# Optimization experiments

Hardware: AMD Instinct MI355X
Metric: run time of the kernel (lower is better)

The kernel has to match this reference:

```python
import jax, jax.numpy as jnp
import numpy as np

EMBED = 512
H = 8
HD = EMBED // H           # 64
NUM_CLS = 4
WIN = 32                  # one-sided window radius
DIL = 1
WLEN = 2 * WIN + 1        # 65
CTX = NUM_CLS + WLEN      # 69
PATCH_LEN = 8192
B = 1
S = NUM_CLS + PATCH_LEN
THETA = 10000.0
COORD_HIGH = 100000.0
NEG = -1e30


def _rotate_half(x):
    # [..., x1, x2, ...] -> [..., -x2, x1, ...]
    x1 = x[..., 0::2]
    x2 = x[..., 1::2]
    return jnp.stack([-x2, x1], axis=-1).reshape(x.shape)


def _rope2d(x, coords):
    # x: (B,H,L,HD), coords: (B,L,2)
    half = HD // 2
    inv_freq = 1.0 / (THETA ** (jnp.arange(0, half, 2, dtype=jnp.float32) / half))  # (half//2,)
    xy = coords / COORD_HIGH
    fx = xy[..., 0][..., None] * inv_freq   # (B,L,half//2)
    fy = xy[..., 1][..., None] * inv_freq
    fx = jnp.repeat(fx, 2, axis=-1)         # (B,L,half)
    fy = jnp.repeat(fy, 2, axis=-1)
    freqs = jnp.concatenate([fx, fy], axis=-1)[:, None]  # (B,1,L,HD)
    return x * jnp.cos(freqs) + _rotate_half(x) * jnp.sin(freqs)


def setup_inputs() -> dict:
    key = jax.random.key(0)
    k1, k2, k3, k4, k5, k6 = jax.random.split(key, 6)
    x = jax.random.normal(k1, (B, S, EMBED), dtype=jnp.float32)
    coords = jax.random.uniform(k2, (B, PATCH_LEN, 2), dtype=jnp.float32) * COORD_HIGH
    sc = 1.0 / np.sqrt(EMBED)
    w_qkv = jax.random.normal(k3, (3 * EMBED, EMBED), dtype=jnp.float32) * sc
    b_qkv = jax.random.normal(k4, (3 * EMBED,), dtype=jnp.float32) * 0.02
    w_out = jax.random.normal(k5, (EMBED, EMBED), dtype=jnp.float32) * sc
    b_out = jax.random.normal(k6, (EMBED,), dtype=jnp.float32) * 0.02
    return {"x": x, "coords": coords, "w_qkv": w_qkv, "b_qkv": b_qkv,
            "w_out": w_out, "b_out": b_out}


def _forward(x, coords, w_qkv, b_qkv, w_out, b_out):
    Bb, seq_len, _ = x.shape
    qkv = x @ w_qkv.T + b_qkv                       # (B,S,3E)
    qkv = qkv.reshape(Bb, seq_len, 3, H, HD)
    qkv = jnp.transpose(qkv, (2, 0, 3, 1, 4))       # (3,B,H,S,HD)
    q, k, v = qkv[0], qkv[1], qkv[2]
    q_cls, k_cls, v_cls = q[:, :, :NUM_CLS], k[:, :, :NUM_CLS], v[:, :, :NUM_CLS]
    q_p, k_p, v_p = q[:, :, NUM_CLS:], k[:, :, NUM_CLS:], v[:, :, NUM_CLS:]

    q_p = _rope2d(q_p, coords)
    k_p = _rope2d(k_p, coords)
    k_all = jnp.concatenate([k_cls, k_p], axis=2)
    v_all = v

    scale = 1.0 / np.sqrt(HD)

    # --- global CLS attention: CLS queries attend to everything ---
    cls_scores = jnp.einsum('bhqd,bhkd->bhqk', q_cls, k_all) * scale
    cls_probs = jax.nn.softmax(cls_scores, axis=-1)
    cls_out = jnp.einsum('bhqk,bhkd->bhqd', cls_probs, v_all)

    # --- windowed patch attention: patch i -> [CLS | patches i-W..i+W (dilated)] ---
    L = PATCH_LEN
    pad = WIN * DIL
    k_pad = jnp.pad(k_p, ((0, 0), (0, 0), (pad, pad), (0, 0)))
    v_pad = jnp.pad(v_p, ((0, 0), (0, 0), (pad, pad), (0, 0)))
    gather_idx = jnp.arange(L)[:, None] + jnp.arange(WLEN)[None, :] * DIL  # (L,WLEN)
    k_win = k_pad[:, :, gather_idx]   # (B,H,L,WLEN,HD)
    v_win = v_pad[:, :, gather_idx]

    s_cls = jnp.einsum('bhld,bhcd->bhlc', q_p, k_cls) * scale     # (B,H,L,NUM_CLS)
    s_win = jnp.einsum('bhld,bhlwd->bhlw', q_p, k_win) * scale    # (B,H,L,WLEN)

    pos = jnp.arange(L)[:, None] + (jnp.arange(WLEN)[None, :] - WIN) * DIL
    in_bounds = (pos >= 0) & (pos < L)                            # (L,WLEN)
    s_win = jnp.where(in_bounds[None, None], s_win, NEG)

    scores = jnp.concatenate([s_cls, s_win], axis=-1)             # (B,H,L,CTX)
    probs = jax.nn.softmax(scores, axis=-1)
    p_cls, p_win = probs[..., :NUM_CLS], probs[..., NUM_CLS:]
    patch_out = (jnp.einsum('bhlc,bhcd->bhld', p_cls, v_cls)
                 + jnp.einsum('bhlw,bhlwd->bhld', p_win, v_win))

    out = jnp.concatenate([cls_out, patch_out], axis=2)           # (B,H,S,HD)
    out = jnp.transpose(out, (0, 2, 1, 3)).reshape(Bb, seq_len, EMBED)
    return out @ w_out.T + b_out


def reference(x, coords, w_qkv, b_qkv, w_out, b_out):
    return _forward(x, coords, w_qkv, b_qkv, w_out, b_out)
```

## Files before the change

### kernel.cpp

```cpp
#include <hip/hip_runtime.h>
#include <math.h>

#define EMBED 512
#define NHEAD 8
#define HD 64
#define NUM_CLS 4
#define WIN 32
#define WLEN 65
#define PATCH_LEN 8192
#define S_TOT 8196
#define QKV_LD 1536
#define VT_LD 8200

typedef short bf16x8 __attribute__((ext_vector_type(8)));
typedef float f32x4 __attribute__((ext_vector_type(4)));

__device__ __forceinline__ unsigned short f2bf(float f) {
    unsigned u = __float_as_uint(f);
    return (unsigned short)((u + 0x7fffu + ((u >> 16) & 1u)) >> 16);
}
__device__ __forceinline__ float bf2f(unsigned short v) {
    return __uint_as_float((unsigned)v << 16);
}
__device__ __forceinline__ void gll16(const unsigned short* g, unsigned short* l) {
    __builtin_amdgcn_global_load_lds((const __attribute__((address_space(1))) void*)g,
                                     (__attribute__((address_space(3))) void*)l, 16, 0, 0);
}

__global__ __launch_bounds__(256) void cast_all(const float* __restrict__ x,
                                                const float* __restrict__ wq,
                                                const float* __restrict__ wo,
                                                unsigned short* __restrict__ xb,
                                                unsigned short* __restrict__ wqb,
                                                unsigned short* __restrict__ wob)
{
    const int n1 = S_TOT * EMBED;
    const int n2 = 3 * EMBED * EMBED;
    const int n3 = EMBED * EMBED;
    const int i = (blockIdx.x * 256 + threadIdx.x) * 4;
    const float* src;
    unsigned short* dst;
    int j;
    if (i < n1)           { src = x;  dst = xb;  j = i; }
    else if (i < n1 + n2) { src = wq; dst = wqb; j = i - n1; }
    else if (i < n1 + n2 + n3) { src = wo; dst = wob; j = i - n1 - n2; }
    else return;
    const float4 v = *(const float4*)(src + j);
    ushort4 o;
    o.x = f2bf(v.x); o.y = f2bf(v.y); o.z = f2bf(v.z); o.w = f2bf(v.w);
    *(ushort4*)(dst + j) = o;
}

#define EXW 136
__global__ __launch_bounds__(256) void gemm_qkv(const unsigned short* __restrict__ A,
                                                const unsigned short* __restrict__ B,
                                                const float* __restrict__ bias,
                                                unsigned short* __restrict__ C,
                                                const float* __restrict__ coords,
                                                unsigned short* __restrict__ vT)
{
    const int M = S_TOT, N = 3 * EMBED, K = EMBED;
    __shared__ __align__(16) unsigned short SMEM[16384];
    unsigned short* EX = SMEM;

    const int tid = threadIdx.x;
    const int lane = tid & 63, w = tid >> 6;
    const int xcd = blockIdx.x & 7;
    const int s = blockIdx.x >> 3;
    const int bm = xcd + 8 * (s / 12);
    const int bn = s % 12;
    if (bm >= 65) return;

    const int ar0 = tid >> 2;
    const int col8 = (tid & 3) * 8;
    int gm0 = bm * 128 + ar0;       if (gm0 >= M) gm0 = M - 1;
    int gm1 = bm * 128 + ar0 + 64;  if (gm1 >= M) gm1 = M - 1;
    const unsigned short* pa0 = A + (size_t)gm0 * K + col8;
    const unsigned short* pa1 = A + (size_t)gm1 * K + col8;
    const unsigned short* pb0 = B + (size_t)(bn * 128 + ar0) * K + col8;
    const unsigned short* pb1 = B + (size_t)(bn * 128 + ar0 + 64) * K + col8;

    const int wr = (w & 1) * 64;
    const int wc = (w >> 1) * 64;
    const int fr = lane & 15;
    const int fk = (lane >> 4) * 8;

    f32x4 acc[4][4];
#pragma unroll
    for (int mi = 0; mi < 4; ++mi)
#pragma unroll
        for (int ni = 0; ni < 4; ++ni) acc[mi][ni] = (f32x4)0.f;

    gll16(pa0, SMEM + tid * 8);
    gll16(pa1, SMEM + (tid + 256) * 8);
    gll16(pb0, SMEM + 8192 + tid * 8);
    gll16(pb1, SMEM + 8192 + (tid + 256) * 8);

    for (int it = 0; it < 16; ++it) {
        __syncthreads();
        if (it + 1 < 16) {
            const int k0 = (it + 1) * 32;
            const int off = ((it + 1) & 1) * 4096;
            gll16(pa0 + k0, SMEM + off + tid * 8);
            gll16(pa1 + k0, SMEM + off + (tid + 256) * 8);
            gll16(pb0 + k0, SMEM + 8192 + off + tid * 8);
            gll16(pb1 + k0, SMEM + 8192 + off + (tid + 256) * 8);
        }
        const unsigned short* Asb = SMEM + (it & 1) * 4096;
        const unsigned short* Bsb = SMEM + 8192 + (it & 1) * 4096;
        bf16x8 af[4], bf[4];
#pragma unroll
        for (int mi = 0; mi < 4; ++mi)
            af[mi] = *(const bf16x8*)(Asb + (wr + mi * 16 + fr) * 32 + fk);
#pragma unroll
        for (int ni = 0; ni < 4; ++ni)
            bf[ni] = *(const bf16x8*)(Bsb + (wc + ni * 16 + fr) * 32 + fk);
#pragma unroll
        for (int mi = 0; mi < 4; ++mi)
#pragma unroll
            for (int ni = 0; ni < 4; ++ni)
                acc[mi][ni] = __builtin_amdgcn_mfma_f32_16x16x32_bf16(af[mi], bf[ni], acc[mi][ni], 0, 0, 0);
    }
    __syncthreads();

    const int ccol = bn * 128 + wc + fr;

    if (bn < 8) {
        ushort2* rt = (ushort2*)EX;
        for (int idx = tid; idx < 4096; idx += 256) {
            const int rr = idx >> 5, pr = idx & 31;
            int l = bm * 128 + rr - NUM_CLS;
            l = l < 0 ? 0 : (l > PATCH_LEN - 1 ? PATCH_LEN - 1 : l);
            const float cxy = coords[l * 2 + (pr >> 4)] * 1e-5f;
            const float f = cxy * __expf(-(float)(pr & 15) * 0.5756462732485114f);
            float sn, cs;
            __sincosf(f, &sn, &cs);
            ushort2 e; e.x = f2bf(cs); e.y = f2bf(sn);
            rt[idx] = e;
        }
        __syncthreads();

        unsigned pv[4][4][2];
#pragma unroll
        for (int mi = 0; mi < 4; ++mi) {
#pragma unroll
            for (int r = 0; r < 4; ++r) {
                const int rloc = wr + mi * 16 + (lane >> 4) * 4 + r;
                const int row = bm * 128 + rloc;
                const bool patch = (row >= NUM_CLS) && (row < M);
#pragma unroll
                for (int ni = 0; ni < 4; ++ni) {
                    const int col = ccol + ni * 16;
                    const float biased = acc[mi][ni][r] + bias[col];
                    const float prt = __shfl_xor(biased, 1);
                    float outv = biased;
                    if (patch) {
                        const ushort2 e = rt[rloc * 32 + ((col & 63) >> 1)];
                        const float cs = bf2f(e.x), sn = bf2f(e.y);
                        outv = (col & 1) ? (biased * cs + prt * sn)
                                         : (biased * cs - prt * sn);
                    }
                    const unsigned us = f2bf(outv);
                    if (r & 1) pv[mi][ni][r >> 1] |= us << 16;
                    else       pv[mi][ni][r >> 1] = us;
                }
            }
        }
        for (int p = 0; p < 2; ++p) {
            __syncthreads();
            if ((w & 1) == p) {
#pragma unroll
                for (int mi = 0; mi < 4; ++mi) {
#pragma unroll
                    for (int r = 0; r < 4; ++r) {
                        const int rl = mi * 16 + (lane >> 4) * 4 + r;
#pragma unroll
                        for (int ni = 0; ni < 4; ++ni) {
                            const unsigned pw = pv[mi][ni][r >> 1];
                            EX[rl * EXW + wc + fr + ni * 16] =
                                (unsigned short)((r & 1) ? (pw >> 16) : (pw & 0xffff));
                        }
                    }
                }
            }
            __syncthreads();
#pragma unroll
            for (int i = 0; i < 4; ++i) {
                const int idx = tid + 256 * i;
                const int rowl = idx >> 4, ch = idx & 15;
                const int grow = bm * 128 + p * 64 + rowl;
                if (grow < M)
                    *(bf16x8*)(C + (size_t)grow * N + bn * 128 + ch * 8) =
                        *(const bf16x8*)(EX + rowl * EXW + ch * 8);
            }
        }
    } else {
        const int dbase = (bn - 8) * 128;
#pragma unroll
        for (int mi = 0; mi < 4; ++mi) {
            const int rbase = bm * 128 + wr + mi * 16 + (lane >> 4) * 4;
#pragma unroll
            for (int ni = 0; ni < 4; ++ni) {
                const int col = ccol + ni * 16;
#pragma unroll
                for (int r = 0; r < 4; ++r) {
                    const int row = rbase + r;
                    if (row < M)
                        C[(size_t)row * N + col] = f2bf(acc[mi][ni][r] + bias[col]);
                }
            }
        }
        for (int p = 0; p < 2; ++p) {
            __syncthreads();
            if ((w >> 1) == p) {
#pragma unroll
                for (int mi = 0; mi < 4; ++mi) {
                    const int tok0 = wr + mi * 16 + (lane >> 4) * 4;
                    const int rw = bm * 128 + tok0;
#pragma unroll
                    for (int ni = 0; ni < 4; ++ni) {
                        const int col = ccol + ni * 16;
                        const int dloc = fr + 16 * ni;
                        ushort4 o;
                        o.x = (rw + 0 < M) ? f2bf(acc[mi][ni][0] + bias[col]) : (unsigned short)0;
                        o.y = (rw + 1 < M) ? f2bf(acc[mi][ni][1] + bias[col]) : (unsigned short)0;
                        o.z = (rw + 2 < M) ? f2bf(acc[mi][ni][2] + bias[col]) : (unsigned short)0;
                        o.w = (rw + 3 < M) ? f2bf(acc[mi][ni][3] + bias[col]) : (unsigned short)0;
                        *(ushort4*)(EX + dloc * EXW + tok0) = o;
                    }
                }
            }
            __syncthreads();
            const int d = tid >> 2;
            const int tch = (tid & 3) * 32;
            const int gtok = bm * 128 + tch;
            unsigned short* dst = vT + (size_t)(dbase + p * 64 + d) * VT_LD + gtok;
            const unsigned short* srcl = EX + d * EXW + tch;
            if (gtok + 32 <= VT_LD) {
#pragma unroll
                for (int c2 = 0; c2 < 32; c2 += 8)
                    *(bf16x8*)(dst + c2) = *(const bf16x8*)(srcl + c2);
            } else {
                for (int c2 = 0; c2 < 32; ++c2)
                    if (gtok + c2 < VT_LD) dst[c2] = srcl[c2];
            }
        }
    }
}

__global__ __launch_bounds__(256) void gemm_out(const unsigned short* __restrict__ A,
                                                const unsigned short* __restrict__ B,
                                                const float* __restrict__ bias,
                                                float* __restrict__ C)
{
    const int M = S_TOT, N = EMBED, K = EMBED;
    __shared__ __align__(16) unsigned short As[2][64 * 32];
    __shared__ __align__(16) unsigned short Bs[2][128 * 32];
    const int tid = threadIdx.x;
    const int lane = tid & 63, w = tid >> 6;
    const int bn = blockIdx.x, bm = blockIdx.y;

    const int ar0 = tid >> 2;
    const int col8 = (tid & 3) * 8;
    int gm0 = bm * 64 + ar0;  if (gm0 >= M) gm0 = M - 1;
    const unsigned short* pa0 = A + (size_t)gm0 * K + col8;
    const unsigned short* pb0 = B + (size_t)(bn * 128 + ar0) * K + col8;
    const unsigned short* pb1 = B + (size_t)(bn * 128 + ar0 + 64) * K + col8;

    const int wr = (w & 1) * 32;
    const int wc = (w >> 1) * 64;
    const int fr = lane & 15;
    const int fk = (lane >> 4) * 8;

    f32x4 acc[2][4];
#pragma unroll
    for (int mi = 0; mi < 2; ++mi)
#pragma unroll
        for (int ni = 0; ni < 4; ++ni) acc[mi][ni] = (f32x4)0.f;

    gll16(pa0, As[0] + tid * 8);
    gll16(pb0, Bs[0] + tid * 8);
    gll16(pb1, Bs[0] + (tid + 256) * 8);

    for (int it = 0; it < 16; ++it) {
        __syncthreads();
        if (it + 1 < 16) {
            const int k0 = (it + 1) * 32;
            const int nb = (it + 1) & 1;
            gll16(pa0 + k0, As[nb] + tid * 8);
            gll16(pb0 + k0, Bs[nb] + tid * 8);
            gll16(pb1 + k0, Bs[nb] + (tid + 256) * 8);
        }
        const int cb = it & 1;
        bf16x8 af[2], bf[4];
#pragma unroll
        for (int mi = 0; mi < 2; ++mi)
            af[mi] = *(const bf16x8*)(As[cb] + (wr + mi * 16 + fr) * 32 + fk);
#pragma unroll
        for (int ni = 0; ni < 4; ++ni)
            bf[ni] = *(const bf16x8*)(Bs[cb] + (wc + ni * 16 + fr) * 32 + fk);
#pragma unroll
        for (int mi = 0; mi < 2; ++mi)
#pragma unroll
            for (int ni = 0; ni < 4; ++ni)
                acc[mi][ni] = __builtin_amdgcn_mfma_f32_16x16x32_bf16(af[mi], bf[ni], acc[mi][ni], 0, 0, 0);
    }

    const int ccol = bn * 128 + wc + fr;
#pragma unroll
    for (int mi = 0; mi < 2; ++mi) {
        const int rbase = bm * 64 + wr + mi * 16 + (lane >> 4) * 4;
#pragma unroll
        for (int r = 0; r < 4; ++r) {
            const int row = rbase + r;
            if (row < M) {
#pragma unroll
                for (int ni = 0; ni < 4; ++ni)
                    C[(size_t)row * N + ccol + ni * 16] = acc[mi][ni][r] + bias[ccol + ni * 16];
            }
        }
    }
}

#define CCH 128
#define NCHUNK ((S_TOT + CCH - 1) / CCH)
#define PSTRIDE 68

__global__ __launch_bounds__(256) void cls_attn_partial(const unsigned short* __restrict__ qkv,
                                                        float* __restrict__ part)
{
    const int h = blockIdx.x;
    const int c = blockIdx.y;
    const int tid = threadIdx.x;
    const int base = c * CCH;

    __shared__ float qs[4][64];
    __shared__ __align__(16) unsigned short Kl[128 * 64];
    __shared__ float sc[4][CCH];
    __shared__ float ored[4][4][64];
    __shared__ float ml[4][2];

    {
        const int qi = tid >> 6, d = tid & 63;
        qs[qi][d] = bf2f(qkv[(size_t)qi * QKV_LD + h * HD + d]);
    }
    for (int i = tid; i < 1024; i += 256) {
        const int kr = i >> 3;
        const int dc = (i & 7) ^ (kr & 7);
        int j = base + kr; if (j > S_TOT - 1) j = S_TOT - 1;
        gll16(qkv + (size_t)j * QKV_LD + EMBED + h * HD + dc * 8, Kl + i * 8);
    }
    __syncthreads();

    {
        const int jj = tid & 127;
        const int qp = (tid >> 7) * 2;
        const int j = base + jj;
        float s0 = -INFINITY, s1 = -INFINITY;
        if (j < S_TOT) {
            float a0 = 0.f, a1 = 0.f;
#pragma unroll
            for (int cch = 0; cch < 8; ++cch) {
                const int slot = cch ^ (jj & 7);
                const bf16x8 kv8 = *(const bf16x8*)(Kl + jj * 64 + slot * 8);
#pragma unroll
                for (int u = 0; u < 8; ++u) {
                    const float kf = bf2f((unsigned short)kv8[u]);
                    a0 += qs[qp + 0][cch * 8 + u] * kf;
                    a1 += qs[qp + 1][cch * 8 + u] * kf;
                }
            }
            s0 = a0 * 0.125f; s1 = a1 * 0.125f;
        }
        sc[qp + 0][jj] = s0;
        sc[qp + 1][jj] = s1;
    }
    __syncthreads();

    const int w = tid >> 6, lane = tid & 63;
    {
        float m = fmaxf(sc[w][lane], sc[w][lane + 64]);
#pragma unroll
        for (int off = 32; off > 0; off >>= 1) m = fmaxf(m, __shfl_xor(m, off, 64));
        const float e0 = expf(sc[w][lane] - m);
        const float e1 = expf(sc[w][lane + 64] - m);
        sc[w][lane] = e0; sc[w][lane + 64] = e1;
        float lsum = e0 + e1;
#pragma unroll
        for (int off = 32; off > 0; off >>= 1) lsum += __shfl_xor(lsum, off, 64);
        if (lane == 0) { ml[w][0] = m; ml[w][1] = lsum; }
    }
    __syncthreads();

    {
        const int g = w, d = lane;
        float a0 = 0.f, a1 = 0.f, a2 = 0.f, a3 = 0.f;
        for (int jj = g; jj < CCH; jj += 4) {
            const int j = base + jj;
            if (j >= S_TOT) break;
            const float vv = bf2f(qkv[(size_t)j * QKV_LD + 2 * EMBED + h * HD + d]);
            a0 += sc[0][jj] * vv; a1 += sc[1][jj] * vv;
            a2 += sc[2][jj] * vv; a3 += sc[3][jj] * vv;
        }
        ored[g][0][d] = a0; ored[g][1][d] = a1; ored[g][2][d] = a2; ored[g][3][d] = a3;
    }
    __syncthreads();

    {
        const int qi = tid >> 6, d = tid & 63;
        const float o = ored[0][qi][d] + ored[1][qi][d] + ored[2][qi][d] + ored[3][qi][d];
        float* pb = part + ((size_t)(h * NCHUNK + c) * 4 + qi) * PSTRIDE;
        pb[d] = o;
        if (d == 0) { pb[64] = ml[qi][0]; pb[65] = ml[qi][1]; }
    }
}

__global__ __launch_bounds__(256) void cls_attn_combine(const float* __restrict__ part,
                                                        unsigned short* __restrict__ attn)
{
    const int h = blockIdx.x;
    const int qi = threadIdx.x >> 6, d = threadIdx.x & 63;
    float M = -INFINITY;
    for (int c = 0; c < NCHUNK; ++c)
        M = fmaxf(M, part[((size_t)(h * NCHUNK + c) * 4 + qi) * PSTRIDE + 64]);
    float acc = 0.f, L = 0.f;
    for (int c = 0; c < NCHUNK; ++c) {
        const float* pb = part + ((size_t)(h * NCHUNK + c) * 4 + qi) * PSTRIDE;
        const float s = expf(pb[64] - M);
        acc += s * pb[d];
        L   += s * pb[65];
    }
    attn[(size_t)qi * EMBED + h * HD + d] = f2bf(acc / L);
}

#define SW 116
#define PW 136

__global__ __launch_bounds__(256) void patch_attn_mfma(
    const unsigned short* __restrict__ qkv,
    const unsigned short* __restrict__ vT,
    unsigned short* __restrict__ attnb)
{
    const int l0 = blockIdx.x * 32;
    const int h = blockIdx.y;
    const int tid = threadIdx.x;
    const int lane = tid & 63, w = tid >> 6;

    __shared__ __align__(16) unsigned short Qs[32 * 64];
    __shared__ __align__(16) unsigned short Ks[112 * 64];
    __shared__ __align__(16) unsigned short Vt[64 * 128];
    __shared__ __align__(16) float Sm[32 * SW];

    {
        const int i = tid;
        const int t = i >> 3;
        const int dcl = (i & 7) ^ (t & 7);
        gll16(qkv + (size_t)(NUM_CLS + l0 + t) * QKV_LD + h * HD + dcl * 8, Qs + i * 8);
    }
    for (int i = tid; i < 896; i += 256) {
        const int c = i >> 3;
        const int dcl = (i & 7) ^ (c & 7);
        int tok = (c >= 104 && c < 108) ? (c - 104) : (l0 - 32 + c);
        tok = tok < 0 ? 0 : (tok > S_TOT - 1 ? S_TOT - 1 : tok);
        gll16(qkv + (size_t)tok * QKV_LD + EMBED + h * HD + dcl * 8, Ks + i * 8);
    }
    for (int i = tid; i < 1024; i += 256) {
        const int d = i >> 4;
        const int kcl = (i & 15) ^ (d & 15);
        const int c0 = kcl * 8;
        int tokb = (c0 == 104) ? 0 : (l0 - 32 + c0);
        tokb = tokb < 0 ? 0 : (tokb > 8192 ? 8192 : tokb);
        gll16(vT + (size_t)(h * HD + d) * VT_LD + tokb, Vt + i * 8);
    }
    __syncthreads();

    bf16x8 qf[2][2];
#pragma unroll
    for (int mt = 0; mt < 2; ++mt)
#pragma unroll
        for (int ks = 0; ks < 2; ++ks) {
            const int row = mt * 16 + (lane & 15);
            const int dc = (ks * 4 + (lane >> 4)) ^ (row & 7);
            qf[mt][ks] = *(const bf16x8*)(Qs + row * 64 + dc * 8);
        }
    for (int idx = w; idx < 14; idx += 4) {
        const int mt = idx & 1, nt = idx >> 1;
        f32x4 acc = (f32x4)0.f;
#pragma unroll
        for (int ks = 0; ks < 2; ++ks) {
            const int kr = nt * 16 + (lane & 15);
            const int dc = (ks * 4 + (lane >> 4)) ^ (kr & 7);
            const bf16x8 kf = *(const bf16x8*)(Ks + kr * 64 + dc * 8);
            acc = __builtin_amdgcn_mfma_f32_16x16x32_bf16(qf[mt][ks], kf, acc, 0, 0, 0);
        }
        const int col = nt * 16 + (lane & 15);
        const int r0 = mt * 16 + (lane >> 4) * 4;
#pragma unroll
        for (int r = 0; r < 4; ++r) Sm[(r0 + r) * SW + col] = acc[r];
    }
    __syncthreads();

    {
        const int t = tid >> 3, lq = tid & 7;
        float e[14];
        float m = -INFINITY;
#pragma unroll
        for (int j = 0; j < 14; ++j) {
            const int c = lq + 8 * j;
            bool valid;
            if (c >= 104) valid = (c < 108);
            else {
                const int r = c - 4;
                const int pos = l0 - 32 + r;
                valid = (c >= 4) && (c < 100) && (r >= t) && (r <= t + 64) &&
                        (pos >= 0) && (pos < PATCH_LEN);
            }
            e[j] = valid ? Sm[t * SW + c] * 0.125f : -INFINITY;
            m = fmaxf(m, e[j]);
        }
#pragma unroll
        for (int off = 1; off < 8; off <<= 1) m = fmaxf(m, __shfl_xor(m, off, 64));
        float sum = 0.f;
#pragma unroll
        for (int j = 0; j < 14; ++j) { e[j] = expf(e[j] - m); sum += e[j]; }
#pragma unroll
        for (int off = 1; off < 8; off <<= 1) sum += __shfl_xor(sum, off, 64);
        const float inv = 1.f / sum;
        __syncthreads();
        unsigned short* P = (unsigned short*)Sm;
#pragma unroll
        for (int j = 0; j < 14; ++j) P[t * PW + lq + 8 * j] = f2bf(e[j] * inv);
        ushort2 z; z.x = 0; z.y = 0;
        *(ushort2*)(P + (tid >> 3) * PW + 112 + (tid & 7) * 2) = z;
    }
    __syncthreads();

    {
        const unsigned short* P = (const unsigned short*)Sm;
        const int mt = w & 1;
        bf16x8 pf[4];
#pragma unroll
        for (int ks = 0; ks < 4; ++ks) {
            const int row = mt * 16 + (lane & 15);
            pf[ks] = *(const bf16x8*)(P + row * PW + ks * 32 + (lane >> 4) * 8);
        }
#pragma unroll
        for (int nn = 0; nn < 2; ++nn) {
            const int nt = (w >> 1) + nn * 2;
            f32x4 acc = (f32x4)0.f;
#pragma unroll
            for (int ks = 0; ks < 4; ++ks) {
                const int d = nt * 16 + (lane & 15);
                const int kc = (ks * 4 + (lane >> 4)) ^ (d & 15);
                const bf16x8 vf = *(const bf16x8*)(Vt + d * 128 + kc * 8);
                acc = __builtin_amdgcn_mfma_f32_16x16x32_bf16(pf[ks], vf, acc, 0, 0, 0);
            }
            const int dcol = nt * 16 + (lane & 15);
            const int r0 = mt * 16 + (lane >> 4) * 4;
#pragma unroll
            for (int r = 0; r < 4; ++r)
                attnb[(size_t)(NUM_CLS + l0 + r0 + r) * EMBED + h * HD + dcol] = f2bf(acc[r]);
        }
    }
}

extern "C" void kernel_launch(void* const* d_in, const int* in_sizes, int n_in,
                              void* d_out, int out_size, void* d_ws, size_t ws_size,
                              hipStream_t stream)
{
    const float* x      = (const float*)d_in[0];
    const float* coords = (const float*)d_in[1];
    const float* w_qkv  = (const float*)d_in[2];
    const float* b_qkv  = (const float*)d_in[3];
    const float* w_out  = (const float*)d_in[4];
    const float* b_out  = (const float*)d_in[5];
    float* out = (float*)d_out;

    char* p = (char*)d_ws;
    unsigned short* qkv   = (unsigned short*)p;  p += (size_t)S_TOT * QKV_LD * 2;
    unsigned short* vT    = (unsigned short*)p;  p += (size_t)EMBED * VT_LD * 2;
    unsigned short* attnb = (unsigned short*)p;  p += (size_t)S_TOT * EMBED * 2;
    float*          part  = (float*)p;           p += (size_t)NHEAD * NCHUNK * 4 * PSTRIDE * 4;
    unsigned short* wob   = (unsigned short*)p;  p += (size_t)EMBED * EMBED * 2;
    unsigned short* xb    = (unsigned short*)p;  p += (size_t)S_TOT * EMBED * 2;
    unsigned short* wqb   = (unsigned short*)p;


    {
        const int total = S_TOT * EMBED + 3 * EMBED * EMBED + EMBED * EMBED;
        cast_all<<<(total / 4 + 255) / 256, 256, 0, stream>>>(x, w_qkv, w_out, xb, wqb, wob);
    }

    gemm_qkv<<<864, 256, 0, stream>>>(xb, wqb, b_qkv, qkv, coords, vT);

    cls_attn_partial<<<dim3(NHEAD, NCHUNK), 256, 0, stream>>>(qkv, part);
    cls_attn_combine<<<NHEAD, 256, 0, stream>>>(part, attnb);

    patch_attn_mfma<<<dim3(PATCH_LEN / 32, NHEAD), 256, 0, stream>>>(qkv, vT, attnb);

    gemm_out<<<dim3(4, 129), 256, 0, stream>>>(attnb, wob, b_out, out);
}
```

Baseline: 185.0 us.

## Fuse x bf16 cast into QKV GEMM and merge cls/patch attention launches

The QKV GEMM now reads fp32 x directly, converts it to bf16 in registers and stores it to LDS after the MFMAs. This removes the separate cast pass over x and its bf16 workspace copy, but the A loads become register-staged instead of async LDS loads. The patch-attention and cls-partial kernels are merged into one launch with a block-index split, cutting one launch and letting both run concurrently. Weights are still cast in a smaller kernel.

```diff
diff --git a/kernel.cpp b/kernel.cpp
--- a/kernel.cpp
+++ b/kernel.cpp
@@ -26,24 +26,28 @@
     __builtin_amdgcn_global_load_lds((const __attribute__((address_space(1))) void*)g,
                                      (__attribute__((address_space(3))) void*)l, 16, 0, 0);
 }
-
-__global__ __launch_bounds__(256) void cast_all(const float* __restrict__ x,
-                                                const float* __restrict__ wq,
-                                                const float* __restrict__ wo,
-                                                unsigned short* __restrict__ xb,
-                                                unsigned short* __restrict__ wqb,
-                                                unsigned short* __restrict__ wob)
+__device__ __forceinline__ bf16x8 pack8(float4 lo, float4 hi) {
+    bf16x8 r;
+    r[0] = (short)f2bf(lo.x); r[1] = (short)f2bf(lo.y);
+    r[2] = (short)f2bf(lo.z); r[3] = (short)f2bf(lo.w);
+    r[4] = (short)f2bf(hi.x); r[5] = (short)f2bf(hi.y);
+    r[6] = (short)f2bf(hi.z); r[7] = (short)f2bf(hi.w);
+    return r;
+}
+
+__global__ __launch_bounds__(256) void cast_w(const float* __restrict__ wq,
+                                              const float* __restrict__ wo,
+                                              unsigned short* __restrict__ wqb,
+                                              unsigned short* __restrict__ wob)
 {
-    const int n1 = S_TOT * EMBED;
     const int n2 = 3 * EMBED * EMBED;
     const int n3 = EMBED * EMBED;
     const int i = (blockIdx.x * 256 + threadIdx.x) * 4;
     const float* src;
     unsigned short* dst;
     int j;
-    if (i < n1)           { src = x;  dst = xb;  j = i; }
-    else if (i < n1 + n2) { src = wq; dst = wqb; j = i - n1; }
-    else if (i < n1 + n2 + n3) { src = wo; dst = wob; j = i - n1 - n2; }
+    if (i < n2)           { src = wq; dst = wqb; j = i; }
+    else if (i < n2 + n3) { src = wo; dst = wob; j = i - n2; }
     else return;
     const float4 v = *(const float4*)(src + j);
     ushort4 o;
@@ -52,7 +56,7 @@
 }
 
 #define EXW 136
-__global__ __launch_bounds__(256) void gemm_qkv(const unsigned short* __restrict__ A,
+__global__ __launch_bounds__(256) void gemm_qkv(const float* __restrict__ X,
                                                 const unsigned short* __restrict__ B,
                                                 const float* __restrict__ bias,
                                                 unsigned short* __restrict__ C,
@@ -75,8 +79,8 @@
     const int col8 = (tid & 3) * 8;
     int gm0 = bm * 128 + ar0;       if (gm0 >= M) gm0 = M - 1;
     int gm1 = bm * 128 + ar0 + 64;  if (gm1 >= M) gm1 = M - 1;
-    const unsigned short* pa0 = A + (size_t)gm0 * K + col8;
-    const unsigned short* pa1 = A + (size_t)gm1 * K + col8;
+    const float* Xp0 = X + (size_t)gm0 * K + col8;
+    const float* Xp1 = X + (size_t)gm1 * K + col8;
     const unsigned short* pb0 = B + (size_t)(bn * 128 + ar0) * K + col8;
     const unsigned short* pb1 = B + (size_t)(bn * 128 + ar0 + 64) * K + col8;
 
@@ -91,20 +95,30 @@
 #pragma unroll
         for (int ni = 0; ni < 4; ++ni) acc[mi][ni] = (f32x4)0.f;
 
-    gll16(pa0, SMEM + tid * 8);
-    gll16(pa1, SMEM + (tid + 256) * 8);
-    gll16(pb0, SMEM + 8192 + tid * 8);
-    gll16(pb1, SMEM + 8192 + (tid + 256) * 8);
+    {
+        const float4 a00 = *(const float4*)(Xp0);
+        const float4 a01 = *(const float4*)(Xp0 + 4);
+        const float4 a10 = *(const float4*)(Xp1);
+        const float4 a11 = *(const float4*)(Xp1 + 4);
+        gll16(pb0, SMEM + 8192 + tid * 8);
+        gll16(pb1, SMEM + 8192 + (tid + 256) * 8);
+        *(bf16x8*)(SMEM + tid * 8) = pack8(a00, a01);
+        *(bf16x8*)(SMEM + (tid + 256) * 8) = pack8(a10, a11);
+    }
 
     for (int it = 0; it < 16; ++it) {
         __syncthreads();
-        if (it + 1 < 16) {
-            const int k0 = (it + 1) * 32;
+        float4 n00, n01, n10, n11;
+        const bool more = (it + 1 < 16);
+        if (more) {
+            const int kf = (it + 1) * 32;
+            n00 = *(const float4*)(Xp0 + kf);
+            n01 = *(const float4*)(Xp0 + kf + 4);
+            n10 = *(const float4*)(Xp1 + kf);
+            n11 = *(const float4*)(Xp1 + kf + 4);
             const int off = ((it + 1) & 1) * 4096;
-            gll16(pa0 + k0, SMEM + off + tid * 8);
-            gll16(pa1 + k0, SMEM + off + (tid + 256) * 8);
-            gll16(pb0 + k0, SMEM + 8192 + off + tid * 8);
-            gll16(pb1 + k0, SMEM + 8192 + off + (tid + 256) * 8);
+            gll16(pb0 + kf, SMEM + 8192 + off + tid * 8);
+            gll16(pb1 + kf, SMEM + 8192 + off + (tid + 256) * 8);
         }
         const unsigned short* Asb = SMEM + (it & 1) * 4096;
         const unsigned short* Bsb = SMEM + 8192 + (it & 1) * 4096;
@@ -120,6 +134,11 @@
 #pragma unroll
             for (int ni = 0; ni < 4; ++ni)
                 acc[mi][ni] = __builtin_amdgcn_mfma_f32_16x16x32_bf16(af[mi], bf[ni], acc[mi][ni], 0, 0, 0);
+        if (more) {
+            const int off = ((it + 1) & 1) * 4096;
+            *(bf16x8*)(SMEM + off + tid * 8) = pack8(n00, n01);
+            *(bf16x8*)(SMEM + off + (tid + 256) * 8) = pack8(n10, n11);
+        }
     }
     __syncthreads();
 
@@ -325,93 +344,223 @@
 #define CCH 128
 #define NCHUNK ((S_TOT + CCH - 1) / CCH)
 #define PSTRIDE 68
-
-__global__ __launch_bounds__(256) void cls_attn_partial(const unsigned short* __restrict__ qkv,
-                                                        float* __restrict__ part)
+#define SW 116
+#define PW 136
+
+__global__ __launch_bounds__(256) void attn_fused(
+    const unsigned short* __restrict__ qkv,
+    const unsigned short* __restrict__ vT,
+    float* __restrict__ part,
+    unsigned short* __restrict__ attnb)
 {
-    const int h = blockIdx.x;
-    const int c = blockIdx.y;
+    __shared__ __align__(16) char SM[49664];
     const int tid = threadIdx.x;
-    const int base = c * CCH;
-
-    __shared__ float qs[4][64];
-    __shared__ __align__(16) unsigned short Kl[128 * 64];
-    __shared__ float sc[4][CCH];
-    __shared__ float ored[4][4][64];
-    __shared__ float ml[4][2];
-
-    {
-        const int qi = tid >> 6, d = tid & 63;
-        qs[qi][d] = bf2f(qkv[(size_t)qi * QKV_LD + h * HD + d]);
-    }
-    for (int i = tid; i < 1024; i += 256) {
-        const int kr = i >> 3;
-        const int dc = (i & 7) ^ (kr & 7);
-        int j = base + kr; if (j > S_TOT - 1) j = S_TOT - 1;
-        gll16(qkv + (size_t)j * QKV_LD + EMBED + h * HD + dc * 8, Kl + i * 8);
-    }
-    __syncthreads();
-
-    {
-        const int jj = tid & 127;
-        const int qp = (tid >> 7) * 2;
-        const int j = base + jj;
-        float s0 = -INFINITY, s1 = -INFINITY;
-        if (j < S_TOT) {
-            float a0 = 0.f, a1 = 0.f;
-#pragma unroll
-            for (int cch = 0; cch < 8; ++cch) {
-                const int slot = cch ^ (jj & 7);
-                const bf16x8 kv8 = *(const bf16x8*)(Kl + jj * 64 + slot * 8);
-#pragma unroll
-                for (int u = 0; u < 8; ++u) {
-                    const float kf = bf2f((unsigned short)kv8[u]);
-                    a0 += qs[qp + 0][cch * 8 + u] * kf;
-                    a1 += qs[qp + 1][cch * 8 + u] * kf;
+    const int lane = tid & 63, w = tid >> 6;
+
+    if (blockIdx.x < 2048) {
+        const int l0 = (blockIdx.x >> 3) * 32;
+        const int h = blockIdx.x & 7;
+        unsigned short* Qs = (unsigned short*)SM;
+        unsigned short* Ks = (unsigned short*)(SM + 4096);
+        unsigned short* Vt = (unsigned short*)(SM + 18432);
+        float* Sm = (float*)(SM + 34816);
+
+        {
+            const int i = tid;
+            const int t = i >> 3;
+            const int dcl = (i & 7) ^ (t & 7);
+            gll16(qkv + (size_t)(NUM_CLS + l0 + t) * QKV_LD + h * HD + dcl * 8, Qs + i * 8);
+        }
+        for (int i = tid; i < 896; i += 256) {
+            const int c = i >> 3;
+            const int dcl = (i & 7) ^ (c & 7);
+            int tok = (c >= 104 && c < 108) ? (c - 104) : (l0 - 32 + c);
+            tok = tok < 0 ? 0 : (tok > S_TOT - 1 ? S_TOT - 1 : tok);
+            gll16(qkv + (size_t)tok * QKV_LD + EMBED + h * HD + dcl * 8, Ks + i * 8);
+        }
+        for (int i = tid; i < 1024; i += 256) {
+            const int d = i >> 4;
+            const int kcl = (i & 15) ^ (d & 15);
+            const int c0 = kcl * 8;
+            int tokb = (c0 == 104) ? 0 : (l0 - 32 + c0);
+            tokb = tokb < 0 ? 0 : (tokb > 8192 ? 8192 : tokb);
+            gll16(vT + (size_t)(h * HD + d) * VT_LD + tokb, Vt + i * 8);
+        }
+        __syncthreads();
+
+        bf16x8 qf[2][2];
+#pragma unroll
+        for (int mt = 0; mt < 2; ++mt)
+#pragma unroll
+            for (int ks = 0; ks < 2; ++ks) {
+                const int row = mt * 16 + (lane & 15);
+                const int dc = (ks * 4 + (lane >> 4)) ^ (row & 7);
+                qf[mt][ks] = *(const bf16x8*)(Qs + row * 64 + dc * 8);
+            }
+        for (int idx = w; idx < 14; idx += 4) {
+            const int mt = idx & 1, nt = idx >> 1;
+            f32x4 acc = (f32x4)0.f;
+#pragma unroll
+            for (int ks = 0; ks < 2; ++ks) {
+                const int kr = nt * 16 + (lane & 15);
+                const int dc = (ks * 4 + (lane >> 4)) ^ (kr & 7);
+                const bf16x8 kf = *(const bf16x8*)(Ks + kr * 64 + dc * 8);
+                acc = __builtin_amdgcn_mfma_f32_16x16x32_bf16(qf[mt][ks], kf, acc, 0, 0, 0);
+            }
+            const int col = nt * 16 + (lane & 15);
+            const int r0 = mt * 16 + (lane >> 4) * 4;
+#pragma unroll
+            for (int r = 0; r < 4; ++r) Sm[(r0 + r) * SW + col] = acc[r];
+        }
+        __syncthreads();
+
+        {
+            const int t = tid >> 3, lq = tid & 7;
+            float e[14];
+            float m = -INFINITY;
+#pragma unroll
+            for (int j = 0; j < 14; ++j) {
+                const int c = lq + 8 * j;
+                bool valid;
+                if (c >= 104) valid = (c < 108);
+                else {
+                    const int r = c - 4;
+                    const int pos = l0 - 32 + r;
+                    valid = (c >= 4) && (c < 100) && (r >= t) && (r <= t + 64) &&
+                            (pos >= 0) && (pos < PATCH_LEN);
                 }
-            }
-            s0 = a0 * 0.125f; s1 = a1 * 0.125f;
-        }
-        sc[qp + 0][jj] = s0;
-        sc[qp + 1][jj] = s1;
-    }
-    __syncthreads();
-
-    const int w = tid >> 6, lane = tid & 63;
-    {
-        float m = fmaxf(sc[w][lane], sc[w][lane + 64]);
-#pragma unroll
-        for (int off = 32; off > 0; off >>= 1) m = fmaxf(m, __shfl_xor(m, off, 64));
-        const float e0 = expf(sc[w][lane] - m);
-        const float e1 = expf(sc[w][lane + 64] - m);
-        sc[w][lane] = e0; sc[w][lane + 64] = e1;
-        float lsum = e0 + e1;
-#pragma unroll
-        for (int off = 32; off > 0; off >>= 1) lsum += __shfl_xor(lsum, off, 64);
-        if (lane == 0) { ml[w][0] = m; ml[w][1] = lsum; }
-    }
-    __syncthreads();
-
-    {
-        const int g = w, d = lane;
-        float a0 = 0.f, a1 = 0.f, a2 = 0.f, a3 = 0.f;
-        for (int jj = g; jj < CCH; jj += 4) {
+                e[j] = valid ? Sm[t * SW + c] * 0.125f : -INFINITY;
+                m = fmaxf(m, e[j]);
+            }
+#pragma unroll
+            for (int off = 1; off < 8; off <<= 1) m = fmaxf(m, __shfl_xor(m, off, 64));
+            float sum = 0.f;
+#pragma unroll
+            for (int j = 0; j < 14; ++j) { e[j] = expf(e[j] - m); sum += e[j]; }
+#pragma unroll
+            for (int off = 1; off < 8; off <<= 1) sum += __shfl_xor(sum, off, 64);
+            const float inv = 1.f / sum;
+            __syncthreads();
+            unsigned short* P = (unsigned short*)Sm;
+#pragma unroll
+            for (int j = 0; j < 14; ++j) P[t * PW + lq + 8 * j] = f2bf(e[j] * inv);
+            ushort2 z; z.x = 0; z.y = 0;
+            *(ushort2*)(P + (tid >> 3) * PW + 112 + (tid & 7) * 2) = z;
+        }
+        __syncthreads();
+
+        {
+            const unsigned short* P = (const unsigned short*)Sm;
+            const int mt = w & 1;
+            bf16x8 pf[4];
+#pragma unroll
+            for (int ks = 0; ks < 4; ++ks) {
+                const int row = mt * 16 + (lane & 15);
+                pf[ks] = *(const bf16x8*)(P + row * PW + ks * 32 + (lane >> 4) * 8);
+            }
+#pragma unroll
+            for (int nn = 0; nn < 2; ++nn) {
+                const int nt = (w >> 1) + nn * 2;
+                f32x4 acc = (f32x4)0.f;
+#pragma unroll
+                for (int ks = 0; ks < 4; ++ks) {
+                    const int d = nt * 16 + (lane & 15);
+                    const int kc = (ks * 4 + (lane >> 4)) ^ (d & 15);
+                    const bf16x8 vf = *(const bf16x8*)(Vt + d * 128 + kc * 8);
+                    acc = __builtin_amdgcn_mfma_f32_16x16x32_bf16(pf[ks], vf, acc, 0, 0, 0);
+                }
+                const int dcol = nt * 16 + (lane & 15);
+                const int r0 = mt * 16 + (lane >> 4) * 4;
+#pragma unroll
+                for (int r = 0; r < 4; ++r)
+                    attnb[(size_t)(NUM_CLS + l0 + r0 + r) * EMBED + h * HD + dcol] = f2bf(acc[r]);
+            }
+        }
+    } else {
+        const int cid = blockIdx.x - 2048;
+        const int h = cid & 7;
+        const int c = cid >> 3;
+        const int base = c * CCH;
+        float* qs = (float*)SM;
+        unsigned short* Kl = (unsigned short*)(SM + 1024);
+        float* sc = (float*)(SM + 17408);
+        float* ored = (float*)(SM + 19456);
+        float* ml = (float*)(SM + 23552);
+
+        {
+            const int qi = tid >> 6, d = tid & 63;
+            qs[qi * 64 + d] = bf2f(qkv[(size_t)qi * QKV_LD + h * HD + d]);
+        }
+        for (int i = tid; i < 1024; i += 256) {
+            const int kr = i >> 3;
+            const int dc = (i & 7) ^ (kr & 7);
+            int j = base + kr; if (j > S_TOT - 1) j = S_TOT - 1;
+            gll16(qkv + (size_t)j * QKV_LD + EMBED + h * HD + dc * 8, Kl + i * 8);
+        }
+        __syncthreads();
+
+        {
+            const int jj = tid & 127;
+            const int qp = (tid >> 7) * 2;
             const int j = base + jj;
-            if (j >= S_TOT) break;
-            const float vv = bf2f(qkv[(size_t)j * QKV_LD + 2 * EMBED + h * HD + d]);
-            a0 += sc[0][jj] * vv; a1 += sc[1][jj] * vv;
-            a2 += sc[2][jj] * vv; a3 += sc[3][jj] * vv;
-        }
-        ored[g][0][d] = a0; ored[g][1][d] = a1; ored[g][2][d] = a2; ored[g][3][d] = a3;
-    }
-    __syncthreads();
-
-    {
-        const int qi = tid >> 6, d = tid & 63;
-        const float o = ored[0][qi][d] + ored[1][qi][d] + ored[2][qi][d] + ored[3][qi][d];
-        float* pb = part + ((size_t)(h * NCHUNK + c) * 4 + qi) * PSTRIDE;
-        pb[d] = o;
-        if (d == 0) { pb[64] = ml[qi][0]; pb[65] = ml[qi][1]; }
+            float s0 = -INFINITY, s1 = -INFINITY;
+            if (j < S_TOT) {
+                float a0 = 0.f, a1 = 0.f;
+#pragma unroll
+                for (int cch = 0; cch < 8; ++cch) {
+                    const int slot = cch ^ (jj & 7);
+                    const bf16x8 kv8 = *(const bf16x8*)(Kl + jj * 64 + slot * 8);
+#pragma unroll
+                    for (int u = 0; u < 8; ++u) {
+                        const float kf = bf2f((unsigned short)kv8[u]);
+                        a0 += qs[(qp + 0) * 64 + cch * 8 + u] * kf;
+                        a1 += qs[(qp + 1) * 64 + cch * 8 + u] * kf;
+                    }
+                }
+                s0 = a0 * 0.125f; s1 = a1 * 0.125f;
+            }
+            sc[(qp + 0) * CCH + jj] = s0;
+            sc[(qp + 1) * CCH + jj] = s1;
+        }
+        __syncthreads();
+
+        {
+            float m = fmaxf(sc[w * CCH + lane], sc[w * CCH + lane + 64]);
+#pragma unroll
+            for (int off = 32; off > 0; off >>= 1) m = fmaxf(m, __shfl_xor(m, off, 64));
+            const float e0 = expf(sc[w * CCH + lane] - m);
+            const float e1 = expf(sc[w * CCH + lane + 64] - m);
+            sc[w * CCH + lane] = e0; sc[w * CCH + lane + 64] = e1;
+            float lsum = e0 + e1;
+#pragma unroll
+            for (int off = 32; off > 0; off >>= 1) lsum += __shfl_xor(lsum, off, 64);
+            if (lane == 0) { ml[w * 2 + 0] = m; ml[w * 2 + 1] = lsum; }
+        }
+        __syncthreads();
+
+        {
+            const int g = w, d = lane;
+            float a0 = 0.f, a1 = 0.f, a2 = 0.f, a3 = 0.f;
+            for (int jj = g; jj < CCH; jj += 4) {
+                const int j = base + jj;
+                if (j >= S_TOT) break;
+                const float vv = bf2f(qkv[(size_t)j * QKV_LD + 2 * EMBED + h * HD + d]);
+                a0 += sc[0 * CCH + jj] * vv; a1 += sc[1 * CCH + jj] * vv;
+                a2 += sc[2 * CCH + jj] * vv; a3 += sc[3 * CCH + jj] * vv;
+            }
+            ored[(g * 4 + 0) * 64 + d] = a0; ored[(g * 4 + 1) * 64 + d] = a1;
+            ored[(g * 4 + 2) * 64 + d] = a2; ored[(g * 4 + 3) * 64 + d] = a3;
+        }
+        __syncthreads();
+
+        {
+            const int qi = tid >> 6, d = tid & 63;
+            const float o = ored[(0 * 4 + qi) * 64 + d] + ored[(1 * 4 + qi) * 64 + d] +
+                            ored[(2 * 4 + qi) * 64 + d] + ored[(3 * 4 + qi) * 64 + d];
+            float* pb = part + ((size_t)(h * NCHUNK + c) * 4 + qi) * PSTRIDE;
+            pb[d] = o;
+            if (d == 0) { pb[64] = ml[qi * 2 + 0]; pb[65] = ml[qi * 2 + 1]; }
+        }
     }
 }
 
@@ -433,137 +582,6 @@
     attn[(size_t)qi * EMBED + h * HD + d] = f2bf(acc / L);
 }
 
-#define SW 116
-#define PW 136
-
-__global__ __launch_bounds__(256) void patch_attn_mfma(
-    const unsigned short* __restrict__ qkv,
-    const unsigned short* __restrict__ vT,
-    unsigned short* __restrict__ attnb)
-{
-    const int l0 = blockIdx.x * 32;
-    const int h = blockIdx.y;
-    const int tid = threadIdx.x;
-    const int lane = tid & 63, w = tid >> 6;
-
-    __shared__ __align__(16) unsigned short Qs[32 * 64];
-    __shared__ __align__(16) unsigned short Ks[112 * 64];
-    __shared__ __align__(16) unsigned short Vt[64 * 128];
-    __shared__ __align__(16) float Sm[32 * SW];
-
-    {
-        const int i = tid;
-        const int t = i >> 3;
-        const int dcl = (i & 7) ^ (t & 7);
-        gll16(qkv + (size_t)(NUM_CLS + l0 + t) * QKV_LD + h * HD + dcl * 8, Qs + i * 8);
-    }
-    for (int i = tid; i < 896; i += 256) {
-        const int c = i >> 3;
-        const int dcl = (i & 7) ^ (c & 7);
-        int tok = (c >= 104 && c < 108) ? (c - 104) : (l0 - 32 + c);
-        tok = tok < 0 ? 0 : (tok > S_TOT - 1 ? S_TOT - 1 : tok);
-        gll16(qkv + (size_t)tok * QKV_LD + EMBED + h * HD + dcl * 8, Ks + i * 8);
-    }
-    for (int i = tid; i < 1024; i += 256) {
-        const int d = i >> 4;
-        const int kcl = (i & 15) ^ (d & 15);
-        const int c0 = kcl * 8;
-        int tokb = (c0 == 104) ? 0 : (l0 - 32 + c0);
-        tokb = tokb < 0 ? 0 : (tokb > 8192 ? 8192 : tokb);
-        gll16(vT + (size_t)(h * HD + d) * VT_LD + tokb, Vt + i * 8);
-    }
-    __syncthreads();
-
-    bf16x8 qf[2][2];
-#pragma unroll
-    for (int mt = 0; mt < 2; ++mt)
-#pragma unroll
-        for (int ks = 0; ks < 2; ++ks) {
-            const int row = mt * 16 + (lane & 15);
-            const int dc = (ks * 4 + (lane >> 4)) ^ (row & 7);
-            qf[mt][ks] = *(const bf16x8*)(Qs + row * 64 + dc * 8);
-        }
-    for (int idx = w; idx < 14; idx += 4) {
-        const int mt = idx & 1, nt = idx >> 1;
-        f32x4 acc = (f32x4)0.f;
-#pragma unroll
-        for (int ks = 0; ks < 2; ++ks) {
-            const int kr = nt * 16 + (lane & 15);
-            const int dc = (ks * 4 + (lane >> 4)) ^ (kr & 7);
-            const bf16x8 kf = *(const bf16x8*)(Ks + kr * 64 + dc * 8);
-            acc = __builtin_amdgcn_mfma_f32_16x16x32_bf16(qf[mt][ks], kf, acc, 0, 0, 0);
-        }
-        const int col = nt * 16 + (lane & 15);
-        const int r0 = mt * 16 + (lane >> 4) * 4;
-#pragma unroll
-        for (int r = 0; r < 4; ++r) Sm[(r0 + r) * SW + col] = acc[r];
-    }
-    __syncthreads();
-
-    {
-        const int t = tid >> 3, lq = tid & 7;
-        float e[14];
-        float m = -INFINITY;
-#pragma unroll
-        for (int j = 0; j < 14; ++j) {
-            const int c = lq + 8 * j;
-            bool valid;
-            if (c >= 104) valid = (c < 108);
-            else {
-                const int r = c - 4;
-                const int pos = l0 - 32 + r;
-                valid = (c >= 4) && (c < 100) && (r >= t) && (r <= t + 64) &&
-                        (pos >= 0) && (pos < PATCH_LEN);
-            }
-            e[j] = valid ? Sm[t * SW + c] * 0.125f : -INFINITY;
-            m = fmaxf(m, e[j]);
-        }
-#pragma unroll
-        for (int off = 1; off < 8; off <<= 1) m = fmaxf(m, __shfl_xor(m, off, 64));
-        float sum = 0.f;
-#pragma unroll
-        for (int j = 0; j < 14; ++j) { e[j] = expf(e[j] - m); sum += e[j]; }
-#pragma unroll
-        for (int off = 1; off < 8; off <<= 1) sum += __shfl_xor(sum, off, 64);
-        const float inv = 1.f / sum;
-        __syncthreads();
-        unsigned short* P = (unsigned short*)Sm;
-#pragma unroll
-        for (int j = 0; j < 14; ++j) P[t * PW + lq + 8 * j] = f2bf(e[j] * inv);
-        ushort2 z; z.x = 0; z.y = 0;
-        *(ushort2*)(P + (tid >> 3) * PW + 112 + (tid & 7) * 2) = z;
-    }
-    __syncthreads();
-
-    {
-        const unsigned short* P = (const unsigned short*)Sm;
-        const int mt = w & 1;
-        bf16x8 pf[4];
-#pragma unroll
-        for (int ks = 0; ks < 4; ++ks) {
-            const int row = mt * 16 + (lane & 15);
-            pf[ks] = *(const bf16x8*)(P + row * PW + ks * 32 + (lane >> 4) * 8);
-        }
-#pragma unroll
-        for (int nn = 0; nn < 2; ++nn) {
-            const int nt = (w >> 1) + nn * 2;
-            f32x4 acc = (f32x4)0.f;
-#pragma unroll
-            for (int ks = 0; ks < 4; ++ks) {
-                const int d = nt * 16 + (lane & 15);
-                const int kc = (ks * 4 + (lane >> 4)) ^ (d & 15);
-                const bf16x8 vf = *(const bf16x8*)(Vt + d * 128 + kc * 8);
-                acc = __builtin_amdgcn_mfma_f32_16x16x32_bf16(pf[ks], vf, acc, 0, 0, 0);
-            }
-            const int dcol = nt * 16 + (lane & 15);
-            const int r0 = mt * 16 + (lane >> 4) * 4;
-#pragma unroll
-            for (int r = 0; r < 4; ++r)
-                attnb[(size_t)(NUM_CLS + l0 + r0 + r) * EMBED + h * HD + dcol] = f2bf(acc[r]);
-        }
-    }
-}
-
 extern "C" void kernel_launch(void* const* d_in, const int* in_sizes, int n_in,
                               void* d_out, int out_size, void* d_ws, size_t ws_size,
                               hipStream_t stream)
@@ -582,21 +600,16 @@
     unsigned short* attnb = (unsigned short*)p;  p += (size_t)S_TOT * EMBED * 2;
     float*          part  = (float*)p;           p += (size_t)NHEAD * NCHUNK * 4 * PSTRIDE * 4;
     unsigned short* wob   = (unsigned short*)p;  p += (size_t)EMBED * EMBED * 2;
-    unsigned short* xb    = (unsigned short*)p;  p += (size_t)S_TOT * EMBED * 2;
     unsigned short* wqb   = (unsigned short*)p;
 
 
-    {
-        const int total = S_TOT * EMBED + 3 * EMBED * EMBED + EMBED * EMBED;
-        cast_all<<<(total / 4 + 255) / 256, 256, 0, stream>>>(x, w_qkv, w_out, xb, wqb, wob);
-    }
-
-    gemm_qkv<<<864, 256, 0, stream>>>(xb, wqb, b_qkv, qkv, coords, vT);
-
-    cls_attn_partial<<<dim3(NHEAD, NCHUNK), 256, 0, stream>>>(qkv, part);
+    cast_w<<<1024, 256, 0, stream>>>(w_qkv, w_out, wqb, wob);
+
+    gemm_qkv<<<864, 256, 0, stream>>>(x, wqb, b_qkv, qkv, coords, vT);
+
+    attn_fused<<<2048 + NHEAD * NCHUNK, 256, 0, stream>>>(qkv, vT, part, attnb);
+
     cls_attn_combine<<<NHEAD, 256, 0, stream>>>(part, attnb);
 
-    patch_attn_mfma<<<dim3(PATCH_LEN / 32, NHEAD), 256, 0, stream>>>(qkv, vT, attnb);
-
     gemm_out<<<dim3(4, 129), 256, 0, stream>>>(attnb, wob, b_out, out);
 }
```

Result: faster. 180.5 us (-2.4%).
